# Kernel optimization log

Hardware: AMD Instinct MI355X
Metric: run time of the kernel (lower is better)

## Reference

```python
import jax, jax.numpy as jnp
import numpy as np

IN_FEATURES = 48
OUT_FEATURES = 64
ALPHA = 0.2  # LeakyReLU negative slope
NUM_INTENT = 16
N = 8192


def setup_inputs() -> dict:
    key = jax.random.key(0)
    k1, k2, k3, k4, k5 = jax.random.split(key, 5)
    # Xavier-uniform-ish params (exact init doesn't matter for correctness testing)
    W = jax.random.uniform(k1, (IN_FEATURES, OUT_FEATURES), jnp.float32, -0.3, 0.3)
    a = jax.random.uniform(k2, (2 * OUT_FEATURES, 1), jnp.float32, -0.3, 0.3)
    intent_interaction = jax.random.normal(k3, (NUM_INTENT, NUM_INTENT), jnp.float32) * 0.1
    intent_alpha = jnp.asarray(0.1, jnp.float32)
    inp = jax.random.normal(k4, (N, IN_FEATURES), jnp.float32)
    adj = jnp.ones((N, N), jnp.float32)  # unused by the math, kept for signature fidelity
    intent_labels = jax.random.randint(k5, (N,), 0, NUM_INTENT, jnp.int64 if jax.config.jax_enable_x64 else jnp.int32)
    return {"input": inp, "adj": adj, "W": W, "a": a,
            "intent_interaction": intent_interaction, "intent_alpha": intent_alpha,
            "intent_labels": intent_labels}


def reference(input, adj, W, a, intent_interaction, intent_alpha, intent_labels):
    h = input @ W                       # [N, F]
    F_ = h.shape[1]
    a1 = a[:F_, 0]                      # source part of attention vector
    a2 = a[F_:, 0]                      # target part
    # e[i,j] = leakyrelu(a1.h_i + a2.h_j) without materializing [N,N,2F]
    s1 = h @ a1                         # [N]
    s2 = h @ a2                         # [N]
    spatial_e = jax.nn.leaky_relu(s1[:, None] + s2[None, :], negative_slope=ALPHA)
    # intent bias: gather from interaction matrix, no python loops
    idx = jnp.clip(intent_labels - 1, 0, NUM_INTENT - 1)
    intent_bias = intent_interaction[idx[:, None], idx[None, :]]  # [N, N]
    total_e = spatial_e + intent_alpha * intent_bias
    # NOTE: original softmaxes over dim=0 (columns) and does NOT mask with adj
    attention = jax.nn.softmax(total_e, axis=0)
    h_prime = attention @ h             # [N, F]
    return jax.nn.elu(h_prime)          # concat=True path
```

## Files before the change

kernel.cpp:

```cpp
#include <hip/hip_runtime.h>

#define NN 8192
#define FF 64
#define INF 48
#define NC 16
#define CAP 2048
#define LOG2E 1.4426950408889634f

__device__ __forceinline__ float fexp2(float x) { return __builtin_amdgcn_exp2f(x); }
__device__ __forceinline__ float elu(float v) { return v > 0.f ? v : __expf(v) - 1.f; }

__global__ __launch_bounds__(256) void k1(const float* __restrict__ in,
                                          const float* __restrict__ W,
                                          const float* __restrict__ a,
                                          const int* __restrict__ labels,
                                          float* __restrict__ h,
                                          float* __restrict__ s1L,
                                          float* __restrict__ s2L,
                                          int* __restrict__ ci) {
  __shared__ float sIn[4][INF];
  int t = threadIdx.x;
  int w = t >> 6, lane = t & 63;
  int i = blockIdx.x * 4 + w;
  if (lane < INF) sIn[w][lane] = in[i * INF + lane];
  __syncthreads();
  float acc = 0.f;
#pragma unroll
  for (int k = 0; k < INF; k++) acc += sIn[w][k] * W[k * FF + lane];
  h[i * FF + lane] = acc;
  float v1 = acc * a[lane];
  float v2 = acc * a[FF + lane];
#pragma unroll
  for (int off = 32; off > 0; off >>= 1) {
    v1 += __shfl_xor(v1, off, 64);
    v2 += __shfl_xor(v2, off, 64);
  }
  if (lane == 0) {
    s1L[i] = v1 * LOG2E;
    s2L[i] = v2 * LOG2E;
    int c = labels[i] - 1;
    ci[i] = c < 0 ? 0 : (c > 15 ? 15 : c);
  }
}

__global__ __launch_bounds__(1024) void k2(const float* __restrict__ s1L,
                                           const float* __restrict__ s2L,
                                           const int* __restrict__ ci,
                                           int* __restrict__ offG,
                                           float* __restrict__ s1s,
                                           float* __restrict__ sufA,
                                           float* __restrict__ preB,
                                           float* __restrict__ s2s,
                                           int* __restrict__ perm2,
                                           float* __restrict__ ea2,
                                           float* __restrict__ eb2) {
  __shared__ int wcnt[16][16];
  __shared__ int tot[16];
  __shared__ int offL[17];
  __shared__ int idxL[CAP];
  __shared__ float key[CAP];
  __shared__ int pay[CAP];
  __shared__ float exA[CAP];
  __shared__ float exB[CAP];
  __shared__ float wred[32];
  __shared__ float wexA[17], wexB[17];
  __shared__ int gcnt;
  int t = threadIdx.x;
  int wv = t >> 6, lane = t & 63;
  int myc = blockIdx.x >> 1;
  int half = blockIdx.x & 1;
  unsigned long long lower = (1ULL << lane) - 1ULL;
  int c8[8];
#pragma unroll
  for (int k = 0; k < 8; k++) c8[k] = ci[wv * 512 + k * 64 + lane];
  if (t == 0) gcnt = 0;
#pragma unroll 1
  for (int cls = 0; cls < 16; cls++) {
    int run = 0;
#pragma unroll
    for (int k = 0; k < 8; k++) run += __popcll(__ballot(c8[k] == cls));
    if (lane == 0) wcnt[wv][cls] = run;
  }
  __syncthreads();
  if (t < 16) {
    int s = 0;
#pragma unroll
    for (int w = 0; w < 16; w++) s += wcnt[w][t];
    tot[t] = s;
  }
  __syncthreads();
  if (t == 0) {
    int s = 0;
    for (int c = 0; c < 16; c++) { offL[c] = s; s += tot[c]; }
    offL[16] = s;
  }
  __syncthreads();
  if (blockIdx.x == 0 && t < 17) offG[t] = offL[t];
  int moff = offL[myc], msz = tot[myc];
  int offE = moff + myc;
#pragma unroll
  for (int k = 0; k < 8; k++) {
    bool is = (c8[k] == myc);
    unsigned long long m = __ballot(is);
    int cnt = __popcll(m);
    int base = 0;
    if (lane == 0 && cnt) base = atomicAdd(&gcnt, cnt);
    base = __shfl(base, 0, 64);
    if (is) idxL[base + __popcll(m & lower)] = wv * 512 + k * 64 + lane;
  }
  __syncthreads();
  const float* src = (half == 0) ? s1L : s2L;
  bool fast = (msz <= 1024);
  if (half == 0) {
    if (fast) {
      float v = (t < msz) ? src[idxL[t]] : 3.0e38f;
#pragma unroll
      for (int kk = 2; kk <= 64; kk <<= 1) {
#pragma unroll
        for (int jj = kk >> 1; jj > 0; jj >>= 1) {
          bool sel = ((t & kk) == 0) == ((t & jj) == 0);
          float pv = __shfl_xor(v, jj, 64);
          v = sel ? fminf(v, pv) : fmaxf(v, pv);
        }
      }
      key[t] = v;
      __syncthreads();
      for (int kk = 128; kk <= 1024; kk <<= 1) {
        for (int jj = kk >> 1; jj >= 64; jj >>= 1) {
          int l = t ^ jj;
          if (l > t) {
            float av = key[t], bv = key[l];
            if ((av > bv) == ((t & kk) == 0)) { key[t] = bv; key[l] = av; }
          }
          __syncthreads();
        }
        v = key[t];
        bool up = ((t & kk) == 0);
#pragma unroll
        for (int jj = 32; jj > 0; jj >>= 1) {
          bool sel = up == ((t & jj) == 0);
          float pv = __shfl_xor(v, jj, 64);
          v = sel ? fminf(v, pv) : fmaxf(v, pv);
        }
        key[t] = v;
        __syncthreads();
      }
    } else {
      key[t] = (t < msz) ? src[idxL[t]] : 3.0e38f;
      key[t + 1024] = (t + 1024 < msz) ? src[idxL[t + 1024]] : 3.0e38f;
      __syncthreads();
      float v0 = key[t], v1 = key[t + 1024];
#pragma unroll
      for (int kk = 2; kk <= 64; kk <<= 1) {
#pragma unroll
        for (int jj = kk >> 1; jj > 0; jj >>= 1) {
          bool sel = ((t & kk) == 0) == ((t & jj) == 0);
          float p0 = __shfl_xor(v0, jj, 64);
          float p1 = __shfl_xor(v1, jj, 64);
          v0 = sel ? fminf(v0, p0) : fmaxf(v0, p0);
          v1 = sel ? fminf(v1, p1) : fmaxf(v1, p1);
        }
      }
      key[t] = v0; key[t + 1024] = v1;
      __syncthreads();
      for (int kk = 128; kk <= 2048; kk <<= 1) {
        for (int jj = kk >> 1; jj >= 64; jj >>= 1) {
#pragma unroll
          for (int e2 = 0; e2 < 2; e2++) {
            int e = t + e2 * 1024;
            int l = e ^ jj;
            if (l > e) {
              float av = key[e], bv = key[l];
              if ((av > bv) == ((e & kk) == 0)) { key[e] = bv; key[l] = av; }
            }
          }
          __syncthreads();
        }
        v0 = key[t]; v1 = key[t + 1024];
        bool up0 = ((t & kk) == 0);
        bool up1 = (((t + 1024) & kk) == 0);
#pragma unroll
        for (int jj = 32; jj > 0; jj >>= 1) {
          bool s2b = ((t & jj) == 0);
          float p0 = __shfl_xor(v0, jj, 64);
          float p1 = __shfl_xor(v1, jj, 64);
          v0 = (up0 == s2b) ? fminf(v0, p0) : fmaxf(v0, p0);
          v1 = (up1 == s2b) ? fminf(v1, p1) : fmaxf(v1, p1);
        }
        key[t] = v0; key[t + 1024] = v1;
        __syncthreads();
      }
    }
    for (int m = t; m < CAP; m += 1024) {
      bool in = m < msz;
      float kv = in ? key[m] : 0.f;
      if (in) s1s[moff + m] = kv;
      exA[m] = in ? fexp2(kv) : 0.f;
      exB[m] = in ? fexp2(0.2f * kv) : 0.f;
    }
    __syncthreads();
    float v0 = exA[2 * t], v1 = exA[2 * t + 1];
    float u0 = exB[2 * t], u1 = exB[2 * t + 1];
    float ts = v0 + v1, us = u0 + u1;
    float tsi = ts, usi = us;
#pragma unroll
    for (int d = 1; d < 64; d <<= 1) {
      float nA = __shfl_up(tsi, d, 64);
      float nB = __shfl_up(usi, d, 64);
      if (lane >= d) { tsi += nA; usi += nB; }
    }
    if (lane == 63) { wred[wv] = tsi; wred[16 + wv] = usi; }
    __syncthreads();
    if (t == 0) {
      float sA = 0.f, sB = 0.f;
      for (int w = 0; w < 16; w++) { wexA[w] = sA; wexB[w] = sB; sA += wred[w]; sB += wred[16 + w]; }
      wexA[16] = sA; wexB[16] = sB;
    }
    __syncthreads();
    float eAr = wexA[wv] + (tsi - ts);
    float eBr = wexB[wv] + (usi - us);
    exA[2 * t] = eAr; exA[2 * t + 1] = eAr + v0;
    exB[2 * t] = eBr; exB[2 * t + 1] = eBr + u0;
    __syncthreads();
    float totA = wexA[16];
    for (int k = t; k <= msz; k += 1024) {
      sufA[offE + k] = totA - exA[k];
      preB[offE + k] = exB[k];
    }
  } else {
    if (fast) {
      float v = (t < msz) ? src[idxL[t]] : 3.0e38f;
      int pj = (t < msz) ? idxL[t] : -1;
#pragma unroll
      for (int kk = 2; kk <= 64; kk <<= 1) {
#pragma unroll
        for (int jj = kk >> 1; jj > 0; jj >>= 1) {
          bool sel = ((t & kk) == 0) == ((t & jj) == 0);
          float pv = __shfl_xor(v, jj, 64);
          int pp = __shfl_xor(pj, jj, 64);
          bool take = sel ? (pv < v) : (pv > v);
          if (take) { v = pv; pj = pp; }
        }
      }
      key[t] = v; pay[t] = pj;
      __syncthreads();
      for (int kk = 128; kk <= 1024; kk <<= 1) {
        for (int jj = kk >> 1; jj >= 64; jj >>= 1) {
          int l = t ^ jj;
          if (l > t) {
            float av = key[t], bv = key[l];
            if ((av > bv) == ((t & kk) == 0)) {
              key[t] = bv; key[l] = av;
              int pt = pay[t]; pay[t] = pay[l]; pay[l] = pt;
            }
          }
          __syncthreads();
        }
        v = key[t]; pj = pay[t];
        bool up = ((t & kk) == 0);
#pragma unroll
        for (int jj = 32; jj > 0; jj >>= 1) {
          bool sel = up == ((t & jj) == 0);
          float pv = __shfl_xor(v, jj, 64);
          int pp = __shfl_xor(pj, jj, 64);
          bool take = sel ? (pv < v) : (pv > v);
          if (take) { v = pv; pj = pp; }
        }
        key[t] = v; pay[t] = pj;
        __syncthreads();
      }
    } else {
      key[t] = (t < msz) ? src[idxL[t]] : 3.0e38f;
      pay[t] = (t < msz) ? idxL[t] : -1;
      key[t + 1024] = (t + 1024 < msz) ? src[idxL[t + 1024]] : 3.0e38f;
      pay[t + 1024] = (t + 1024 < msz) ? idxL[t + 1024] : -1;
      __syncthreads();
      float v0 = key[t], v1 = key[t + 1024];
      int p0i = pay[t], p1i = pay[t + 1024];
#pragma unroll
      for (int kk = 2; kk <= 64; kk <<= 1) {
#pragma unroll
        for (int jj = kk >> 1; jj > 0; jj >>= 1) {
          bool sel = ((t & kk) == 0) == ((t & jj) == 0);
          float q0 = __shfl_xor(v0, jj, 64);
          int r0 = __shfl_xor(p0i, jj, 64);
          float q1 = __shfl_xor(v1, jj, 64);
          int r1 = __shfl_xor(p1i, jj, 64);
          bool tk0 = sel ? (q0 < v0) : (q0 > v0);
          bool tk1 = sel ? (q1 < v1) : (q1 > v1);
          if (tk0) { v0 = q0; p0i = r0; }
          if (tk1) { v1 = q1; p1i = r1; }
        }
      }
      key[t] = v0; pay[t] = p0i;
      key[t + 1024] = v1; pay[t + 1024] = p1i;
      __syncthreads();
      for (int kk = 128; kk <= 2048; kk <<= 1) {
        for (int jj = kk >> 1; jj >= 64; jj >>= 1) {
#pragma unroll
          for (int e2 = 0; e2 < 2; e2++) {
            int e = t + e2 * 1024;
            int l = e ^ jj;
            if (l > e) {
              float av = key[e], bv = key[l];
              if ((av > bv) == ((e & kk) == 0)) {
                key[e] = bv; key[l] = av;
                int pt = pay[e]; pay[e] = pay[l]; pay[l] = pt;
              }
            }
          }
          __syncthreads();
        }
        v0 = key[t]; v1 = key[t + 1024];
        p0i = pay[t]; p1i = pay[t + 1024];
        bool up0 = ((t & kk) == 0);
        bool up1 = (((t + 1024) & kk) == 0);
#pragma unroll
        for (int jj = 32; jj > 0; jj >>= 1) {
          bool s2b = ((t & jj) == 0);
          float q0 = __shfl_xor(v0, jj, 64);
          int r0 = __shfl_xor(p0i, jj, 64);
          float q1 = __shfl_xor(v1, jj, 64);
          int r1 = __shfl_xor(p1i, jj, 64);
          bool tk0 = (up0 == s2b) ? (q0 < v0) : (q0 > v0);
          bool tk1 = (up1 == s2b) ? (q1 < v1) : (q1 > v1);
          if (tk0) { v0 = q0; p0i = r0; }
          if (tk1) { v1 = q1; p1i = r1; }
        }
        key[t] = v0; pay[t] = p0i;
        key[t + 1024] = v1; pay[t + 1024] = p1i;
        __syncthreads();
      }
    }
    for (int m = t; m < msz; m += 1024) {
      float kv = key[m];
      s2s[moff + m] = kv;
      perm2[moff + m] = pay[m];
      ea2[moff + m] = fexp2(kv);
      eb2[moff + m] = fexp2(0.2f * kv);
    }
  }
}

__global__ __launch_bounds__(256) void k3p(const float* __restrict__ s2L,
                                           const int* __restrict__ ci,
                                           const int* __restrict__ offG,
                                           const float* __restrict__ s1s,
                                           const float* __restrict__ sufA,
                                           const float* __restrict__ preB,
                                           const int* __restrict__ perm2,
                                           const float* __restrict__ ea2,
                                           const float* __restrict__ eb2,
                                           const float* __restrict__ h,
                                           const float* __restrict__ Bmat,
                                           const float* __restrict__ alphap,
                                           float* __restrict__ hpA,
                                           float* __restrict__ hpB) {
  __shared__ float EBT[256];
  __shared__ int offL[17];
  __shared__ float DinvL[16];
  __shared__ int jL[16];
  int t = threadIdx.x;
  EBT[t] = __expf(alphap[0] * Bmat[t]);
  if (t < 17) offL[t] = offG[t];
  __syncthreads();
  int il = t >> 4, c = t & 15;
  int pos0 = blockIdx.x * 16;
  int j = perm2[pos0 + il];
  float s2v = s2L[j];
  int cj = ci[j];
  int o = offL[c], n = offL[c + 1] - o;
  float keyv = -s2v;
  int lo = 0, len = n;
  while (len > 0) {
    int half = len >> 1;
    int mid = lo + half;
    if (s1s[o + mid] <= keyv) { lo = mid + 1; len -= half + 1; }
    else len = half;
  }
  int b = o + c + lo;
  float term = EBT[c * 16 + cj] * fmaf(fexp2(s2v), sufA[b], fexp2(0.2f * s2v) * preB[b]);
#pragma unroll
  for (int d = 1; d < 16; d <<= 1) term += __shfl_xor(term, d, 64);
  if (c == 0) { DinvL[il] = 1.0f / term; jL[il] = j; }
  __syncthreads();
  int wv = t >> 6, lane = t & 63;
#pragma unroll
  for (int r = 0; r < 4; r++) {
    int rr = wv * 4 + r;
    int pp = pos0 + rr;
    float g = DinvL[rr];
    int jj = jL[rr];
    float hv = h[jj * FF + lane];
    hpA[(size_t)pp * FF + lane] = ea2[pp] * g * hv;
    hpB[(size_t)pp * FF + lane] = eb2[pp] * g * hv;
  }
}

__global__ __launch_bounds__(1024) void k4(const int* __restrict__ offG,
                                           const float* __restrict__ hpA,
                                           const float* __restrict__ hpB,
                                           float* __restrict__ sufG1,
                                           float* __restrict__ preG2) {
  __shared__ float ps[16][64];
  __shared__ int offL[17];
  int t = threadIdx.x;
  int wv = t >> 6, f = t & 63;
  if (t < 17) offL[t] = offG[t];
  __syncthreads();
  int cls = blockIdx.x >> 1, dir = blockIdx.x & 1;
  int o = offL[cls], sz = offL[cls + 1] - o, oE = o + cls;
  int L = (sz + 15) >> 4;
  int m0 = wv * L;
  if (m0 > sz) m0 = sz;
  int m1 = m0 + L;
  if (m1 > sz) m1 = sz;
  const float* src = dir ? hpB : hpA;
  float acc = 0.f;
#pragma unroll 4
  for (int m = m0; m < m1; m++) acc += src[(size_t)(o + m) * FF + f];
  ps[wv][f] = acc;
  __syncthreads();
  if (dir == 0) {
    float run = 0.f;
    for (int w = wv + 1; w < 16; w++) run += ps[w][f];
#pragma unroll 4
    for (int m = m1 - 1; m >= m0; m--) {
      run += src[(size_t)(o + m) * FF + f];
      sufG1[(size_t)(oE + m) * FF + f] = run;
    }
    if (wv == 0) sufG1[(size_t)(oE + sz) * FF + f] = 0.f;
  } else {
    float run = 0.f;
    for (int w = 0; w < wv; w++) run += ps[w][f];
#pragma unroll 4
    for (int m = m0; m < m1; m++) {
      preG2[(size_t)(oE + m) * FF + f] = run;
      run += src[(size_t)(o + m) * FF + f];
    }
    if (wv == 15) preG2[(size_t)(oE + sz) * FF + f] = run;
  }
}

__global__ __launch_bounds__(256) void k5(const float* __restrict__ s1L,
                                          const int* __restrict__ ci,
                                          const int* __restrict__ offG,
                                          const float* __restrict__ s2s,
                                          const float* __restrict__ sufG1,
                                          const float* __restrict__ preG2,
                                          const float* __restrict__ Bmat,
                                          const float* __restrict__ alphap,
                                          float* __restrict__ out) {
  __shared__ float EBT[256];
  __shared__ int offL[17];
  int t = threadIdx.x;
  EBT[t] = __expf(alphap[0] * Bmat[t]);
  if (t < 17) offL[t] = offG[t];
  __syncthreads();
  int wv = t >> 6, l = t & 63;
  int i = blockIdx.x * 4 + wv;
  float s1v = s1L[i];
  int ai = ci[i];
  int lo = 0;
  if (l < 16) {
    int o = offL[l], len = offL[l + 1] - o;
    float keyv = -s1v;
    while (len > 0) {
      int half = len >> 1;
      int mid = lo + half;
      if (s2s[o + mid] <= keyv) { lo = mid + 1; len -= half + 1; }
      else len = half;
    }
  }
  float e1 = fexp2(s1v), e1b = fexp2(0.2f * s1v);
  float acc = 0.f;
#pragma unroll
  for (int c = 0; c < NC; c++) {
    int k = __shfl(lo, c, 64);
    int base = (offL[c] + c + k) * FF + l;
    acc = fmaf(EBT[ai * 16 + c], fmaf(e1, sufG1[base], e1b * preG2[base]), acc);
  }
  out[i * FF + l] = elu(acc);
}

extern "C" void kernel_launch(void* const* d_in, const int* in_sizes, int n_in,
                              void* d_out, int out_size, void* d_ws, size_t ws_size,
                              hipStream_t stream) {
  const float* in = (const float*)d_in[0];
  const float* W = (const float*)d_in[2];
  const float* a = (const float*)d_in[3];
  const float* Bmat = (const float*)d_in[4];
  const float* alpha = (const float*)d_in[5];
  const int* labels = (const int*)d_in[6];
  float* out = (float*)d_out;

  float* ws = (float*)d_ws;
  float* h = ws;
  float* s1L = h + 524288;
  float* s2L = s1L + 8192;
  int* ci = (int*)(s2L + 8192);
  int* offG = ci + 8192;
  float* s1s = (float*)(offG + 32);
  float* sufA = s1s + 8192;
  float* preB = sufA + 8224;
  float* s2s = preB + 8224;
  int* perm2 = (int*)(s2s + 8192);
  float* ea2 = (float*)(perm2 + 8192);
  float* eb2 = ea2 + 8192;
  float* hpA = eb2 + 8192;
  float* hpB = hpA + 524288;
  float* sufG1 = hpB + 524288;
  float* preG2 = sufG1 + 8224 * 64;

  k1<<<2048, 256, 0, stream>>>(in, W, a, labels, h, s1L, s2L, ci);
  k2<<<32, 1024, 0, stream>>>(s1L, s2L, ci, offG, s1s, sufA, preB, s2s, perm2, ea2, eb2);
  k3p<<<512, 256, 0, stream>>>(s2L, ci, offG, s1s, sufA, preB, perm2, ea2, eb2, h, Bmat, alpha, hpA, hpB);
  k4<<<32, 1024, 0, stream>>>(offG, hpA, hpB, sufG1, preG2);
  k5<<<2048, 256, 0, stream>>>(s1L, ci, offG, s2s, sufG1, preG2, Bmat, alpha, out);
}
```

Before: 357.7 us.

## Drop second hp buffer, widen prefix-scan grid, trim bitonic stages to class size

k3p now writes a single scaled h buffer (ea2-weighted). k4 rebuilds the second stream on the fly by multiplying by 2^(-0.8 s2), since eb2 equals ea2 times that factor. This removes a 2 MB write in k3p and the matching read in k4. k4 is split into 128 blocks, one per class, direction and quarter of the features, with 64 row chunks each, so more CUs take part in the scan. The bitonic sort loop in k2 now stops at the next power of two above the class size instead of always running to 1024. The exp2 ratio trick may lose precision or overflow for large-magnitude keys.

```diff
diff --git a/kernel.cpp b/kernel.cpp
--- a/kernel.cpp
+++ b/kernel.cpp
@@ -53,7 +53,7 @@
                                            float* __restrict__ s2s,
                                            int* __restrict__ perm2,
                                            float* __restrict__ ea2,
-                                           float* __restrict__ eb2) {
+                                           float* __restrict__ rr2) {
   __shared__ int wcnt[16][16];
   __shared__ int tot[16];
   __shared__ int offL[17];
@@ -111,6 +111,8 @@
   __syncthreads();
   const float* src = (half == 0) ? s1L : s2L;
   bool fast = (msz <= 1024);
+  int KMAX = 128;
+  while (KMAX < msz) KMAX <<= 1;
   if (half == 0) {
     if (fast) {
       float v = (t < msz) ? src[idxL[t]] : 3.0e38f;
@@ -125,7 +127,7 @@
       }
       key[t] = v;
       __syncthreads();
-      for (int kk = 128; kk <= 1024; kk <<= 1) {
+      for (int kk = 128; kk <= KMAX; kk <<= 1) {
         for (int jj = kk >> 1; jj >= 64; jj >>= 1) {
           int l = t ^ jj;
           if (l > t) {
@@ -244,7 +246,7 @@
       }
       key[t] = v; pay[t] = pj;
       __syncthreads();
-      for (int kk = 128; kk <= 1024; kk <<= 1) {
+      for (int kk = 128; kk <= KMAX; kk <<= 1) {
         for (int jj = kk >> 1; jj >= 64; jj >>= 1) {
           int l = t ^ jj;
           if (l > t) {
@@ -337,7 +339,7 @@
       s2s[moff + m] = kv;
       perm2[moff + m] = pay[m];
       ea2[moff + m] = fexp2(kv);
-      eb2[moff + m] = fexp2(0.2f * kv);
+      rr2[moff + m] = fexp2(-0.8f * kv);
     }
   }
 }
@@ -350,12 +352,10 @@
                                            const float* __restrict__ preB,
                                            const int* __restrict__ perm2,
                                            const float* __restrict__ ea2,
-                                           const float* __restrict__ eb2,
                                            const float* __restrict__ h,
                                            const float* __restrict__ Bmat,
                                            const float* __restrict__ alphap,
-                                           float* __restrict__ hpA,
-                                           float* __restrict__ hpB) {
+                                           float* __restrict__ hp) {
   __shared__ float EBT[256];
   __shared__ int offL[17];
   __shared__ float DinvL[16];
@@ -392,53 +392,58 @@
     float g = DinvL[rr];
     int jj = jL[rr];
     float hv = h[jj * FF + lane];
-    hpA[(size_t)pp * FF + lane] = ea2[pp] * g * hv;
-    hpB[(size_t)pp * FF + lane] = eb2[pp] * g * hv;
+    hp[(size_t)pp * FF + lane] = ea2[pp] * g * hv;
   }
 }
 
 __global__ __launch_bounds__(1024) void k4(const int* __restrict__ offG,
-                                           const float* __restrict__ hpA,
-                                           const float* __restrict__ hpB,
+                                           const float* __restrict__ hp,
+                                           const float* __restrict__ rr2,
                                            float* __restrict__ sufG1,
                                            float* __restrict__ preG2) {
-  __shared__ float ps[16][64];
+  __shared__ float ps[64][16];
   __shared__ int offL[17];
   int t = threadIdx.x;
-  int wv = t >> 6, f = t & 63;
   if (t < 17) offL[t] = offG[t];
   __syncthreads();
-  int cls = blockIdx.x >> 1, dir = blockIdx.x & 1;
+  int b = blockIdx.x;
+  int cls = b >> 3, dir = (b >> 2) & 1, fq = b & 3;
+  int fl = t & 15, ch = t >> 4;
+  int f = fq * 16 + fl;
   int o = offL[cls], sz = offL[cls + 1] - o, oE = o + cls;
-  int L = (sz + 15) >> 4;
-  int m0 = wv * L;
+  int L = (sz + 63) >> 6;
+  int m0 = ch * L;
   if (m0 > sz) m0 = sz;
   int m1 = m0 + L;
   if (m1 > sz) m1 = sz;
-  const float* src = dir ? hpB : hpA;
   float acc = 0.f;
+  if (dir == 0) {
 #pragma unroll 4
-  for (int m = m0; m < m1; m++) acc += src[(size_t)(o + m) * FF + f];
-  ps[wv][f] = acc;
+    for (int m = m0; m < m1; m++) acc += hp[(size_t)(o + m) * FF + f];
+  } else {
+#pragma unroll 4
+    for (int m = m0; m < m1; m++) acc += hp[(size_t)(o + m) * FF + f] * rr2[o + m];
+  }
+  ps[ch][fl] = acc;
   __syncthreads();
   if (dir == 0) {
     float run = 0.f;
-    for (int w = wv + 1; w < 16; w++) run += ps[w][f];
+    for (int w = ch + 1; w < 64; w++) run += ps[w][fl];
 #pragma unroll 4
     for (int m = m1 - 1; m >= m0; m--) {
-      run += src[(size_t)(o + m) * FF + f];
+      run += hp[(size_t)(o + m) * FF + f];
       sufG1[(size_t)(oE + m) * FF + f] = run;
     }
-    if (wv == 0) sufG1[(size_t)(oE + sz) * FF + f] = 0.f;
+    if (ch == 0) sufG1[(size_t)(oE + sz) * FF + f] = 0.f;
   } else {
     float run = 0.f;
-    for (int w = 0; w < wv; w++) run += ps[w][f];
+    for (int w = 0; w < ch; w++) run += ps[w][fl];
 #pragma unroll 4
     for (int m = m0; m < m1; m++) {
       preG2[(size_t)(oE + m) * FF + f] = run;
-      run += src[(size_t)(o + m) * FF + f];
-    }
-    if (wv == 15) preG2[(size_t)(oE + sz) * FF + f] = run;
+      run += hp[(size_t)(o + m) * FF + f] * rr2[o + m];
+    }
+    if (ch == 63) preG2[(size_t)(oE + sz) * FF + f] = run;
   }
 }
 
@@ -506,15 +511,14 @@
   float* s2s = preB + 8224;
   int* perm2 = (int*)(s2s + 8192);
   float* ea2 = (float*)(perm2 + 8192);
-  float* eb2 = ea2 + 8192;
-  float* hpA = eb2 + 8192;
-  float* hpB = hpA + 524288;
-  float* sufG1 = hpB + 524288;
+  float* rr2 = ea2 + 8192;
+  float* hp = rr2 + 8192;
+  float* sufG1 = hp + 524288;
   float* preG2 = sufG1 + 8224 * 64;
 
   k1<<<2048, 256, 0, stream>>>(in, W, a, labels, h, s1L, s2L, ci);
-  k2<<<32, 1024, 0, stream>>>(s1L, s2L, ci, offG, s1s, sufA, preB, s2s, perm2, ea2, eb2);
-  k3p<<<512, 256, 0, stream>>>(s2L, ci, offG, s1s, sufA, preB, perm2, ea2, eb2, h, Bmat, alpha, hpA, hpB);
-  k4<<<32, 1024, 0, stream>>>(offG, hpA, hpB, sufG1, preG2);
+  k2<<<32, 1024, 0, stream>>>(s1L, s2L, ci, offG, s1s, sufA, preB, s2s, perm2, ea2, rr2);
+  k3p<<<512, 256, 0, stream>>>(s2L, ci, offG, s1s, sufA, preB, perm2, ea2, h, Bmat, alpha, hp);
+  k4<<<128, 1024, 0, stream>>>(offG, hp, rr2, sufG1, preG2);
   k5<<<2048, 256, 0, stream>>>(s1L, ci, offG, s2s, sufG1, preG2, Bmat, alpha, out);
 }
```

Result: no change. 350.7 us (-1.9%).
